# Optimization experiments

Hardware: AMD Instinct MI355X
Metric: run time of the kernel (lower is better)

## Reference

```python
import jax, jax.numpy as jnp
import numpy as np

DIM = 256
RES = 64
HEADS = 8
WS = 8            # window_size
CS = (8, 64)      # cross_size (cs1 == W so cross grid broadcasts against window grid)
HEAD_DIM = DIM // HEADS
SCALE = HEAD_DIM ** -0.5


def _partition(x, B, sh, sw):
    # x: [B, L, C] -> [B*heads, H//sh, W//sw, sh*sw, head_dim]
    H = W = RES
    C = DIM
    x = x.reshape(B, H // sh, sh, W // sw, sw, HEADS, HEAD_DIM)
    x = x.transpose(0, 5, 1, 3, 2, 4, 6)
    return x.reshape(B * HEADS, H // sh, W // sw, sh * sw, HEAD_DIM)


def setup_inputs() -> dict:
    key = jax.random.key(0)
    qkv = jax.random.normal(key, (3, 8, RES * RES, DIM), dtype=jnp.float32)
    return {"qkv": qkv}


def reference(qkv) -> jnp.ndarray:
    q, k, v = qkv[0], qkv[1], qkv[2]
    B, L, C = q.shape
    H = W = RES

    qw = _partition(q, B, WS, WS) * SCALE            # [Bh, H/ws, W/ws, ws*ws, hd]
    kc = _partition(k, B, CS[0], CS[1])              # [Bh, H/cs0, 1, cs0*cs1, hd]
    vc = _partition(v, B, CS[0], CS[1])

    # Original einsum 'bhwnc,bqkmc->bhwnm' sums k over its cross-window grid (q,k axes);
    # equivalently pre-sum k over those axes, then contract over head_dim.
    k_sum = kc.sum(axis=(1, 2))                      # [Bh, m, hd]
    attn = jnp.einsum('bhwnc,bmc->bhwnm', qw, k_sum) # [Bh, H/ws, W/ws, n, m]
    attn = jax.nn.softmax(attn, axis=-1)

    # broadcast matmul: vc's cross grid (H/cs0, 1) broadcasts to (H/ws, W/ws)
    x = attn @ vc                                    # [Bh, H/ws, W/ws, n, hd]

    x = x.reshape(B, HEADS, H // WS, W // WS, WS, WS, HEAD_DIM)
    x = x.transpose(0, 2, 4, 3, 5, 1, 6).reshape(B, H, W, C).reshape(B, -1, C)
    return x
```

## Files before the change

kernel.cpp:

```cpp
#include <hip/hip_runtime.h>

#define NB 8
#define L_TOT 4096
#define DIM 256
#define HEADS 8
#define HEAD_DIM 32
#define M_TOT 512
#define SCALE 0.17677669529663687f

typedef float f32x16 __attribute__((ext_vector_type(16)));
typedef short bf16x8 __attribute__((ext_vector_type(8)));

__device__ __forceinline__ unsigned short f2bf(float x) {
    union { float f; unsigned u; } un; un.f = x;
    return (unsigned short)((un.u + 0x7FFFu + ((un.u >> 16) & 1u)) >> 16);
}

__device__ __forceinline__ bf16x8 ld_bf8_lds(const unsigned short* p) {
    union { uint2 u[2]; bf16x8 v; } r;
    r.u[0] = *(const uint2*)(p);
    r.u[1] = *(const uint2*)(p + 4);
    return r.v;
}

__global__ __launch_bounds__(256) void ksum_kernel(const float* __restrict__ k,
                                                   unsigned short* __restrict__ ks) {
    const int bh = blockIdx.x >> 3;
    const int part = blockIdx.x & 7;
    const int b = bh >> 3, head = bh & 7;
    const float* kb = k + (size_t)b * L_TOT * DIM + head * HEAD_DIM;
    for (int idx = threadIdx.x; idx < 64 * 32; idx += 256) {
        const int m = part * 64 + (idx >> 5), c = idx & 31;
        float s = 0.f;
#pragma unroll
        for (int hq = 0; hq < 8; ++hq)
            s += kb[(size_t)(hq * 512 + m) * DIM + c];
        ks[(size_t)bh * (M_TOT * HEAD_DIM) + (size_t)m * 32 + c] = f2bf(s);
    }
}

template <bool USE_WS>
__global__ __launch_bounds__(512) void attn_kernel(const float* __restrict__ q,
                                                   const float* __restrict__ kg,
                                                   const float* __restrict__ v,
                                                   const unsigned short* __restrict__ ks,
                                                   float* __restrict__ out) {
    __shared__ unsigned short smem[USE_WS ? (16512 + 8 * 1152) : (18432 + 8 * 1152)];
    const int tid = threadIdx.x;
    const int wave = tid >> 6;
    const int lane = tid & 63;
    const int ql = lane & 31;
    const int hi = lane >> 5;
    const int bh = blockIdx.x >> 3, h = blockIdx.x & 7;
    const int b = bh >> 3, head = bh & 7;

    const float* vbase = v + ((size_t)b * L_TOT + h * M_TOT) * DIM + head * HEAD_DIM;
    unsigned short* P = smem + (USE_WS ? 16512 : 18432) + wave * 1152;

    if (USE_WS) {
        unsigned short* vT = smem;
        for (int idx = tid; idx < M_TOT * HEAD_DIM; idx += 512) {
            const int m = idx >> 5, c = idx & 31;
            vT[c * 516 + m] = f2bf(vbase[(size_t)m * DIM + c]);
        }
    } else {
        unsigned short* KS = smem;
        const float* kb = kg + (size_t)b * L_TOT * DIM + head * HEAD_DIM;
        for (int idx = tid; idx < M_TOT * HEAD_DIM; idx += 512) {
            const int m = idx >> 5, c = idx & 31;
            float s = 0.f;
#pragma unroll
            for (int hq = 0; hq < 8; ++hq)
                s += kb[(size_t)(hq * 512 + m) * DIM + c];
            KS[m * 36 + c] = f2bf(s);
        }
    }
    __syncthreads();

    const float* qbase = q + (size_t)b * L_TOT * DIM + head * HEAD_DIM;
    float* obase = out + (size_t)b * L_TOT * DIM + head * HEAD_DIM;

    for (int gi = 0; gi < 2; ++gi) {
        const int g = wave * 2 + gi;
        const int w = g >> 1, n0 = (g & 1) * 32;
        const int n = n0 + ql;
        const int Lrow = (h * 8 + (n >> 3)) * 64 + w * 8 + (n & 7);

        bf16x8 qf[2];
        {
            const float* qp = qbase + (size_t)Lrow * DIM;
#pragma unroll
            for (int half = 0; half < 2; ++half) {
                const int c0 = 16 * half + 8 * hi;
                float4 f0 = *(const float4*)(qp + c0);
                float4 f1 = *(const float4*)(qp + c0 + 4);
                bf16x8 t;
                t[0] = (short)f2bf(f0.x * SCALE); t[1] = (short)f2bf(f0.y * SCALE);
                t[2] = (short)f2bf(f0.z * SCALE); t[3] = (short)f2bf(f0.w * SCALE);
                t[4] = (short)f2bf(f1.x * SCALE); t[5] = (short)f2bf(f1.y * SCALE);
                t[6] = (short)f2bf(f1.z * SCALE); t[7] = (short)f2bf(f1.w * SCALE);
                qf[half] = t;
            }
        }

        f32x16 O;
#pragma unroll
        for (int r = 0; r < 16; ++r) O[r] = 0.f;
        float mrun = -3.0e38f, lsum = 0.f;

        for (int ch = 0; ch < 16; ++ch) {
            const int M0 = ch * 32;
            f32x16 S;
#pragma unroll
            for (int r = 0; r < 16; ++r) S[r] = 0.f;
#pragma unroll
            for (int half = 0; half < 2; ++half) {
                bf16x8 A;
                if (USE_WS) {
                    A = *(const bf16x8*)(ks + ((size_t)bh * 512 + M0 + ql) * 32 + 16 * half + 8 * hi);
                } else {
                    const unsigned short* KS = smem;
                    A = ld_bf8_lds(KS + (M0 + ql) * 36 + 16 * half + 8 * hi);
                }
                S = __builtin_amdgcn_mfma_f32_32x32x16_bf16(A, qf[half], S, 0, 0, 0);
            }

            float cmax = S[0];
#pragma unroll
            for (int r = 1; r < 16; ++r) cmax = fmaxf(cmax, S[r]);
            cmax = fmaxf(cmax, __shfl_xor(cmax, 32, 64));
            const float mnew = fmaxf(mrun, cmax);
            const float alpha = __expf(mrun - mnew);
            float ps = 0.f;
            unsigned* Pw = (unsigned*)(P + ql * 36) + 2 * hi;
#pragma unroll
            for (int r8 = 0; r8 < 4; ++r8) {
                const float p0 = __expf(S[4 * r8 + 0] - mnew);
                const float p1 = __expf(S[4 * r8 + 1] - mnew);
                const float p2 = __expf(S[4 * r8 + 2] - mnew);
                const float p3 = __expf(S[4 * r8 + 3] - mnew);
                ps += (p0 + p1) + (p2 + p3);
                Pw[4 * r8]     = (unsigned)f2bf(p0) | ((unsigned)f2bf(p1) << 16);
                Pw[4 * r8 + 1] = (unsigned)f2bf(p2) | ((unsigned)f2bf(p3) << 16);
            }
            ps += __shfl_xor(ps, 32, 64);
            lsum = lsum * alpha + ps;
            mrun = mnew;
#pragma unroll
            for (int r = 0; r < 16; ++r) O[r] *= alpha;

#pragma unroll
            for (int kt = 0; kt < 2; ++kt) {
                const int mk = M0 + 16 * kt + 8 * hi;
                bf16x8 Af;
                if (USE_WS) {
                    const unsigned short* vT = smem;
                    Af = ld_bf8_lds(vT + ql * 516 + mk);
                } else {
                    bf16x8 t;
#pragma unroll
                    for (int j = 0; j < 8; ++j)
                        t[j] = (short)f2bf(vbase[(size_t)(mk + j) * DIM + ql]);
                    Af = t;
                }
                const bf16x8 Bf = ld_bf8_lds(P + ql * 36 + 16 * kt + 8 * hi);
                O = __builtin_amdgcn_mfma_f32_32x32x16_bf16(Af, Bf, O, 0, 0, 0);
            }
        }

        const float inv = 1.f / lsum;
        float* ob = obase + (size_t)Lrow * DIM;
#pragma unroll
        for (int r = 0; r < 16; ++r) {
            const int c = (r & 3) + 8 * (r >> 2) + 4 * hi;
            ob[c] = O[r] * inv;
        }
    }
}

extern "C" void kernel_launch(void* const* d_in, const int* in_sizes, int n_in,
                              void* d_out, int out_size, void* d_ws, size_t ws_size,
                              hipStream_t stream) {
    const float* qkv = (const float*)d_in[0];
    const float* q = qkv;
    const float* k = qkv + (size_t)NB * L_TOT * DIM;
    const float* v = qkv + (size_t)2 * NB * L_TOT * DIM;
    float* out = (float*)d_out;
    const size_t ks_bytes = (size_t)NB * HEADS * M_TOT * HEAD_DIM * 2;
    if (ws_size >= ks_bytes) {
        unsigned short* ks = (unsigned short*)d_ws;
        ksum_kernel<<<dim3(512), dim3(256), 0, stream>>>(k, ks);
        attn_kernel<true><<<dim3(512), dim3(512), 0, stream>>>(q, k, v, ks, out);
    } else {
        attn_kernel<false><<<dim3(512), dim3(512), 0, stream>>>(q, k, v, nullptr, out);
    }
}
```

Measured before the change: 209.2 us.

## Keep P in registers, drop online max, split grid and vectorise loads

```diff
diff --git a/kernel.cpp b/kernel.cpp
--- a/kernel.cpp
+++ b/kernel.cpp
@@ -1,4 +1,5 @@
 #include <hip/hip_runtime.h>
+#include <hip/hip_bf16.h>
 
 #define NB 8
 #define L_TOT 4096
@@ -6,65 +7,75 @@
 #define HEADS 8
 #define HEAD_DIM 32
 #define M_TOT 512
-#define SCALE 0.17677669529663687f
+#define QSCALE (0.17677669529663687f * 1.4426950408889634f)
 
 typedef float f32x16 __attribute__((ext_vector_type(16)));
 typedef short bf16x8 __attribute__((ext_vector_type(8)));
 
-__device__ __forceinline__ unsigned short f2bf(float x) {
-    union { float f; unsigned u; } un; un.f = x;
-    return (unsigned short)((un.u + 0x7FFFu + ((un.u >> 16) & 1u)) >> 16);
-}
+union BF8 { bf16x8 v; unsigned u[4]; uint2 u2[2]; };
 
-__device__ __forceinline__ bf16x8 ld_bf8_lds(const unsigned short* p) {
-    union { uint2 u[2]; bf16x8 v; } r;
-    r.u[0] = *(const uint2*)(p);
-    r.u[1] = *(const uint2*)(p + 4);
-    return r.v;
+__device__ __forceinline__ unsigned cvt2(float lo, float hi) {
+    __hip_bfloat162 h = __float22bfloat162_rn(make_float2(lo, hi));
+    union { __hip_bfloat162 h2; unsigned u; } un;
+    un.h2 = h;
+    return un.u;
 }
 
 __global__ __launch_bounds__(256) void ksum_kernel(const float* __restrict__ k,
                                                    unsigned short* __restrict__ ks) {
-    const int bh = blockIdx.x >> 3;
-    const int part = blockIdx.x & 7;
+    const int blk = blockIdx.x;
+    const int bh = blk >> 4, part = blk & 15;
     const int b = bh >> 3, head = bh & 7;
     const float* kb = k + (size_t)b * L_TOT * DIM + head * HEAD_DIM;
-    for (int idx = threadIdx.x; idx < 64 * 32; idx += 256) {
-        const int m = part * 64 + (idx >> 5), c = idx & 31;
-        float s = 0.f;
+    const int c0 = (threadIdx.x & 7) * 4;
+    const int m = part * 32 + (threadIdx.x >> 3);
+    float4 s = make_float4(0.f, 0.f, 0.f, 0.f);
 #pragma unroll
-        for (int hq = 0; hq < 8; ++hq)
-            s += kb[(size_t)(hq * 512 + m) * DIM + c];
-        ks[(size_t)bh * (M_TOT * HEAD_DIM) + (size_t)m * 32 + c] = f2bf(s);
+    for (int hq = 0; hq < 8; ++hq) {
+        const float4 f = *(const float4*)(kb + (size_t)(hq * 512 + m) * DIM + c0);
+        s.x += f.x; s.y += f.y; s.z += f.z; s.w += f.w;
     }
+    uint2 o;
+    o.x = cvt2(s.x, s.y);
+    o.y = cvt2(s.z, s.w);
+    *(uint2*)(ks + ((size_t)bh * M_TOT + m) * HEAD_DIM + c0) = o;
 }
 
 template <bool USE_WS>
-__global__ __launch_bounds__(512) void attn_kernel(const float* __restrict__ q,
-                                                   const float* __restrict__ kg,
-                                                   const float* __restrict__ v,
-                                                   const unsigned short* __restrict__ ks,
-                                                   float* __restrict__ out) {
-    __shared__ unsigned short smem[USE_WS ? (16512 + 8 * 1152) : (18432 + 8 * 1152)];
+__global__ __launch_bounds__(512, 8) void attn_kernel(const float* __restrict__ q,
+                                                      const float* __restrict__ kg,
+                                                      const float* __restrict__ v,
+                                                      const unsigned short* __restrict__ ks,
+                                                      float* __restrict__ out) {
+    __shared__ unsigned short smem[USE_WS ? (32 * 516) : (32 * 516 + 512 * 36)];
+    unsigned short* vT = smem;
+
     const int tid = threadIdx.x;
     const int wave = tid >> 6;
     const int lane = tid & 63;
     const int ql = lane & 31;
     const int hi = lane >> 5;
-    const int bh = blockIdx.x >> 3, h = blockIdx.x & 7;
+
+    const int bid = blockIdx.x;
+    const int wk = (bid & 7) * 128 + (bid >> 3);
+    const int bh = wk >> 4, h = (wk >> 1) & 7, half = wk & 1;
     const int b = bh >> 3, head = bh & 7;
 
     const float* vbase = v + ((size_t)b * L_TOT + h * M_TOT) * DIM + head * HEAD_DIM;
-    unsigned short* P = smem + (USE_WS ? 16512 : 18432) + wave * 1152;
 
-    if (USE_WS) {
-        unsigned short* vT = smem;
-        for (int idx = tid; idx < M_TOT * HEAD_DIM; idx += 512) {
-            const int m = idx >> 5, c = idx & 31;
-            vT[c * 516 + m] = f2bf(vbase[(size_t)m * DIM + c]);
-        }
-    } else {
-        unsigned short* KS = smem;
+#pragma unroll
+    for (int it = 0; it < 8; ++it) {
+        const int idx = it * 512 + tid;
+        const int m = idx >> 3, c0 = (idx & 7) * 4;
+        const float4 f = *(const float4*)(vbase + (size_t)m * DIM + c0);
+        const unsigned w0 = cvt2(f.x, f.y), w1 = cvt2(f.z, f.w);
+        vT[(c0 + 0) * 516 + m] = (unsigned short)w0;
+        vT[(c0 + 1) * 516 + m] = (unsigned short)(w0 >> 16);
+        vT[(c0 + 2) * 516 + m] = (unsigned short)w1;
+        vT[(c0 + 3) * 516 + m] = (unsigned short)(w1 >> 16);
+    }
+    unsigned short* KS = smem + 32 * 516;
+    if (!USE_WS) {
         const float* kb = kg + (size_t)b * L_TOT * DIM + head * HEAD_DIM;
         for (int idx = tid; idx < M_TOT * HEAD_DIM; idx += 512) {
             const int m = idx >> 5, c = idx & 31;
@@ -72,109 +83,95 @@
 #pragma unroll
             for (int hq = 0; hq < 8; ++hq)
                 s += kb[(size_t)(hq * 512 + m) * DIM + c];
-            KS[m * 36 + c] = f2bf(s);
+            KS[m * 36 + c] = (unsigned short)cvt2(s, 0.f);
         }
     }
     __syncthreads();
 
-    const float* qbase = q + (size_t)b * L_TOT * DIM + head * HEAD_DIM;
-    float* obase = out + (size_t)b * L_TOT * DIM + head * HEAD_DIM;
+    const int g = half * 8 + wave;
+    const int wcol = g >> 1, n0 = (g & 1) * 32;
+    const int n = n0 + ql;
+    const int Lq = (h * 8 + (n >> 3)) * 64 + wcol * 8 + (n & 7);
+    const float* qp = q + ((size_t)b * L_TOT + Lq) * DIM + head * HEAD_DIM;
 
-    for (int gi = 0; gi < 2; ++gi) {
-        const int g = wave * 2 + gi;
-        const int w = g >> 1, n0 = (g & 1) * 32;
-        const int n = n0 + ql;
-        const int Lrow = (h * 8 + (n >> 3)) * 64 + w * 8 + (n & 7);
+    BF8 qf0, qf1;
+    {
+        const float4 f0 = *(const float4*)(qp + 8 * hi);
+        const float4 f1 = *(const float4*)(qp + 8 * hi + 4);
+        qf0.u[0] = cvt2(f0.x * QSCALE, f0.y * QSCALE);
+        qf0.u[1] = cvt2(f0.z * QSCALE, f0.w * QSCALE);
+        qf0.u[2] = cvt2(f1.x * QSCALE, f1.y * QSCALE);
+        qf0.u[3] = cvt2(f1.z * QSCALE, f1.w * QSCALE);
+        const float4 f2 = *(const float4*)(qp + 16 + 8 * hi);
+        const float4 f3 = *(const float4*)(qp + 16 + 8 * hi + 4);
+        qf1.u[0] = cvt2(f2.x * QSCALE, f2.y * QSCALE);
+        qf1.u[1] = cvt2(f2.z * QSCALE, f2.w * QSCALE);
+        qf1.u[2] = cvt2(f3.x * QSCALE, f3.y * QSCALE);
+        qf1.u[3] = cvt2(f3.z * QSCALE, f3.w * QSCALE);
+    }
 
-        bf16x8 qf[2];
-        {
-            const float* qp = qbase + (size_t)Lrow * DIM;
+    const unsigned short* ksb = ks + (size_t)bh * M_TOT * HEAD_DIM;
+
+    f32x16 O;
 #pragma unroll
-            for (int half = 0; half < 2; ++half) {
-                const int c0 = 16 * half + 8 * hi;
-                float4 f0 = *(const float4*)(qp + c0);
-                float4 f1 = *(const float4*)(qp + c0 + 4);
-                bf16x8 t;
-                t[0] = (short)f2bf(f0.x * SCALE); t[1] = (short)f2bf(f0.y * SCALE);
-                t[2] = (short)f2bf(f0.z * SCALE); t[3] = (short)f2bf(f0.w * SCALE);
-                t[4] = (short)f2bf(f1.x * SCALE); t[5] = (short)f2bf(f1.y * SCALE);
-                t[6] = (short)f2bf(f1.z * SCALE); t[7] = (short)f2bf(f1.w * SCALE);
-                qf[half] = t;
-            }
+    for (int r = 0; r < 16; ++r) O[r] = 0.f;
+    float lsum = 0.f;
+
+    for (int ch = 0; ch < 16; ++ch) {
+        const int M0 = ch << 5;
+        f32x16 S;
+#pragma unroll
+        for (int r = 0; r < 16; ++r) S[r] = 0.f;
+
+        BF8 A0, A1;
+        if (USE_WS) {
+            A0.v = *(const bf16x8*)(ksb + (size_t)(M0 + ql) * 32 + 8 * hi);
+            A1.v = *(const bf16x8*)(ksb + (size_t)(M0 + ql) * 32 + 16 + 8 * hi);
+        } else {
+            const unsigned short* kr = KS + (M0 + ql) * 36 + 8 * hi;
+            A0.u2[0] = *(const uint2*)(kr);
+            A0.u2[1] = *(const uint2*)(kr + 4);
+            A1.u2[0] = *(const uint2*)(kr + 16);
+            A1.u2[1] = *(const uint2*)(kr + 20);
         }
+        S = __builtin_amdgcn_mfma_f32_32x32x16_bf16(A0.v, qf0.v, S, 0, 0, 0);
+        S = __builtin_amdgcn_mfma_f32_32x32x16_bf16(A1.v, qf1.v, S, 0, 0, 0);
 
-        f32x16 O;
+        float p[16];
 #pragma unroll
-        for (int r = 0; r < 16; ++r) O[r] = 0.f;
-        float mrun = -3.0e38f, lsum = 0.f;
+        for (int r = 0; r < 16; ++r) p[r] = __builtin_amdgcn_exp2f(S[r]);
+#pragma unroll
+        for (int r = 0; r < 16; ++r) lsum += p[r];
 
-        for (int ch = 0; ch < 16; ++ch) {
-            const int M0 = ch * 32;
-            f32x16 S;
+        unsigned w0 = cvt2(p[0], p[1]),   w1 = cvt2(p[2], p[3]);
+        unsigned w2 = cvt2(p[4], p[5]),   w3 = cvt2(p[6], p[7]);
+        unsigned w4 = cvt2(p[8], p[9]),   w5 = cvt2(p[10], p[11]);
+        unsigned w6 = cvt2(p[12], p[13]), w7 = cvt2(p[14], p[15]);
+        asm("v_permlane32_swap_b32 %0, %1" : "+v"(w0), "+v"(w2));
+        asm("v_permlane32_swap_b32 %0, %1" : "+v"(w1), "+v"(w3));
+        asm("v_permlane32_swap_b32 %0, %1" : "+v"(w4), "+v"(w6));
+        asm("v_permlane32_swap_b32 %0, %1" : "+v"(w5), "+v"(w7));
+        BF8 PA0, PA1, VB0, VB1;
+        PA0.u[0] = w0; PA0.u[1] = w1; PA0.u[2] = w2; PA0.u[3] = w3;
+        PA1.u[0] = w4; PA1.u[1] = w5; PA1.u[2] = w6; PA1.u[3] = w7;
+        const unsigned short* vb = vT + ql * 516 + M0 + 8 * hi;
+        VB0.u2[0] = *(const uint2*)(vb);
+        VB0.u2[1] = *(const uint2*)(vb + 4);
+        VB1.u2[0] = *(const uint2*)(vb + 16);
+        VB1.u2[1] = *(const uint2*)(vb + 20);
+        O = __builtin_amdgcn_mfma_f32_32x32x16_bf16(PA0.v, VB0.v, O, 0, 0, 0);
+        O = __builtin_amdgcn_mfma_f32_32x32x16_bf16(PA1.v, VB1.v, O, 0, 0, 0);
+    }
+
+    lsum += __shfl_xor(lsum, 32, 64);
+    const float inv = __builtin_amdgcn_rcpf(lsum);
+
+    const int rowBase = h * 512 + (n0 >> 3) * 64 + wcol * 8 + 4 * hi;
+    float* ob = out + ((size_t)b * L_TOT + rowBase) * DIM + head * HEAD_DIM + ql;
 #pragma unroll
-            for (int r = 0; r < 16; ++r) S[r] = 0.f;
-#pragma unroll
-            for (int half = 0; half < 2; ++half) {
-                bf16x8 A;
-                if (USE_WS) {
-                    A = *(const bf16x8*)(ks + ((size_t)bh * 512 + M0 + ql) * 32 + 16 * half + 8 * hi);
-                } else {
-                    const unsigned short* KS = smem;
-                    A = ld_bf8_lds(KS + (M0 + ql) * 36 + 16 * half + 8 * hi);
-                }
-                S = __builtin_amdgcn_mfma_f32_32x32x16_bf16(A, qf[half], S, 0, 0, 0);
-            }
-
-            float cmax = S[0];
-#pragma unroll
-            for (int r = 1; r < 16; ++r) cmax = fmaxf(cmax, S[r]);
-            cmax = fmaxf(cmax, __shfl_xor(cmax, 32, 64));
-            const float mnew = fmaxf(mrun, cmax);
-            const float alpha = __expf(mrun - mnew);
-            float ps = 0.f;
-            unsigned* Pw = (unsigned*)(P + ql * 36) + 2 * hi;
-#pragma unroll
-            for (int r8 = 0; r8 < 4; ++r8) {
-                const float p0 = __expf(S[4 * r8 + 0] - mnew);
-                const float p1 = __expf(S[4 * r8 + 1] - mnew);
-                const float p2 = __expf(S[4 * r8 + 2] - mnew);
-                const float p3 = __expf(S[4 * r8 + 3] - mnew);
-                ps += (p0 + p1) + (p2 + p3);
-                Pw[4 * r8]     = (unsigned)f2bf(p0) | ((unsigned)f2bf(p1) << 16);
-                Pw[4 * r8 + 1] = (unsigned)f2bf(p2) | ((unsigned)f2bf(p3) << 16);
-            }
-            ps += __shfl_xor(ps, 32, 64);
-            lsum = lsum * alpha + ps;
-            mrun = mnew;
-#pragma unroll
-            for (int r = 0; r < 16; ++r) O[r] *= alpha;
-
-#pragma unroll
-            for (int kt = 0; kt < 2; ++kt) {
-                const int mk = M0 + 16 * kt + 8 * hi;
-                bf16x8 Af;
-                if (USE_WS) {
-                    const unsigned short* vT = smem;
-                    Af = ld_bf8_lds(vT + ql * 516 + mk);
-                } else {
-                    bf16x8 t;
-#pragma unroll
-                    for (int j = 0; j < 8; ++j)
-                        t[j] = (short)f2bf(vbase[(size_t)(mk + j) * DIM + ql]);
-                    Af = t;
-                }
-                const bf16x8 Bf = ld_bf8_lds(P + ql * 36 + 16 * kt + 8 * hi);
-                O = __builtin_amdgcn_mfma_f32_32x32x16_bf16(Af, Bf, O, 0, 0, 0);
-            }
-        }
-
-        const float inv = 1.f / lsum;
-        float* ob = obase + (size_t)Lrow * DIM;
-#pragma unroll
-        for (int r = 0; r < 16; ++r) {
-            const int c = (r & 3) + 8 * (r >> 2) + 4 * hi;
-            ob[c] = O[r] * inv;
-        }
+    for (int r = 0; r < 16; ++r) {
+        const float iv = __shfl(inv, (r & 3) + 8 * (r >> 2) + 4 * hi, 64);
+        ob[(size_t)((r >> 2) * 64 + (r & 3)) * DIM] = O[r] * iv;
     }
 }
 
@@ -189,9 +186,9 @@
     const size_t ks_bytes = (size_t)NB * HEADS * M_TOT * HEAD_DIM * 2;
     if (ws_size >= ks_bytes) {
         unsigned short* ks = (unsigned short*)d_ws;
-        ksum_kernel<<<dim3(512), dim3(256), 0, stream>>>(k, ks);
-        attn_kernel<true><<<dim3(512), dim3(512), 0, stream>>>(q, k, v, ks, out);
+        ksum_kernel<<<dim3(1024), dim3(256), 0, stream>>>(k, ks);
+        attn_kernel<true><<<dim3(1024), dim3(512), 0, stream>>>(q, k, v, ks, out);
     } else {
-        attn_kernel<false><<<dim3(512), dim3(512), 0, stream>>>(q, k, v, nullptr, out);
+        attn_kernel<false><<<dim3(1024), dim3(512), 0, stream>>>(q, k, v, nullptr, out);
     }
 }
```

New measurement: 178.5 us. -14.7%, faster.
